# Optimization experiments

Hardware: AMD Instinct MI355X
Metric: run time of the kernel (lower is better)

The kernel has to match this reference:

```python
import jax, jax.numpy as jnp
import numpy as np

B, N, D, H = 256, 1000, 512, 8
HD = D // H


def _xavier(key, shape):
    # xavier_uniform-style init (bound = sqrt(6/(fan_in+fan_out)))
    bound = np.sqrt(6.0 / (shape[0] + shape[1])).astype(np.float32)
    return jax.random.uniform(key, shape, jnp.float32, -bound, bound)


def setup_inputs() -> dict:
    key = jax.random.key(0)
    ks = jax.random.split(key, 12)
    encoder_inputs = jax.random.normal(ks[0], (B, N, D), jnp.float32)
    pool = jax.random.normal(ks[1], (B, D), jnp.float32)
    dynamic_capacity = jax.random.uniform(ks[2], (B, 1), jnp.float32)
    mask = jax.random.randint(ks[3], (B, N), 0, 2).astype(jnp.int32)
    mask = mask.at[:, 0].set(0)  # depot always feasible -> MHA softmax well-defined
    return {
        'encoder_inputs': encoder_inputs,
        'pool': pool,
        'dynamic_capacity': dynamic_capacity,
        'mask': mask,
        'W_fc': _xavier(ks[4], (D + 1, D)),   # GAT_Decoder.fc (stored as [in,out])
        'W_fc1': _xavier(ks[5], (D, D)),      # GAT_Decoder.fc1
        'Wq': _xavier(ks[6], (D, D)),         # TransformerAttention.w (cat=1)
        'Wk_mha': _xavier(ks[7], (D, D)),     # TransformerAttention.k
        'Wv': _xavier(ks[8], (D, D)),         # TransformerAttention.v
        'Wo': _xavier(ks[9], (D, D)),         # TransformerAttention.fc
        'Wk_ptr': _xavier(ks[10], (D, D)),    # PointerAttention.k
    }


def reference(encoder_inputs, pool, dynamic_capacity, mask,
              W_fc, W_fc1, Wq, Wk_mha, Wv, Wo, Wk_ptr):
    T = 1.0
    norm_mha = np.float32(1.0 / np.sqrt(HD))
    norm_ptr = np.float32(1.0 / np.sqrt(D))
    mb = mask.astype(bool)                                   # [B,N]

    # --- one decode step of GAT_Decoder ---
    _input = encoder_inputs[:, 0, :]                          # [B,D]
    dec_in = jnp.concatenate([_input, dynamic_capacity], -1)  # [B,D+1]
    state = dec_in @ W_fc + pool @ W_fc1                      # [B,D] (fc + fc1(pool))

    # --- TransformerAttention (single-query masked MHA) ---
    Q = (state @ Wq).reshape(B, H, HD)                        # [B,H,hd]
    K = (encoder_inputs @ Wk_mha).reshape(B, N, H, HD)        # [B,N,H,hd]
    V = (encoder_inputs @ Wv).reshape(B, N, H, HD)
    compat = norm_mha * jnp.einsum('bhd,bnhd->bhn', Q, K)    # [B,H,N]
    u = jnp.where(mb[:, None, :], -jnp.inf, compat)
    attn = jax.nn.softmax(u, axis=-1)                         # [B,H,N]
    mha_out = jnp.einsum('bhn,bnhd->bhd', attn, V).reshape(B, D) @ Wo  # [B,D]

    # --- Pointer attention (tanh-clipped logits) ---
    Kp = encoder_inputs @ Wk_ptr                              # [B,N,D]
    compat2 = norm_ptr * jnp.einsum('bd,bnd->bn', mha_out, Kp)  # [B,N]
    x = jnp.tanh(compat2) * 10.0
    x = jnp.where(mb, -jnp.inf, x)
    all_masked = jnp.all(x == -jnp.inf, axis=-1, keepdims=True)
    x = jnp.where(all_masked, 0.0, x)                         # uniform fallback
    scores = jax.nn.softmax(x / T, axis=-1)                   # [B,N]
    return scores
```

## Files before the change

kernel.cpp:

```cpp
#include <hip/hip_runtime.h>
#include <cstdint>
#include <cstddef>

#define BB 256
#define NN 1000
#define DD 512
#define HH 8

__global__ __launch_bounds__(256) void k_state(
    const float* __restrict__ X, const float* __restrict__ pool,
    const float* __restrict__ cap, const float* __restrict__ Wfc,
    const float* __restrict__ Wfc1, float* __restrict__ state) {
  __shared__ float dec_lds[8][DD];
  __shared__ float pool_lds[8][DD];
  __shared__ float cap_lds[8];
  const int t = threadIdx.x;
  const int b0 = blockIdx.x * 8;
  for (int i = t; i < 8 * 128; i += 256) {
    int r = i >> 7, c4 = i & 127;
    ((float4*)dec_lds[r])[c4]  = ((const float4*)(X + (size_t)(b0 + r) * NN * DD))[c4];
    ((float4*)pool_lds[r])[c4] = ((const float4*)(pool + (size_t)(b0 + r) * DD))[c4];
  }
  if (t < 8) cap_lds[t] = cap[b0 + t];
  __syncthreads();
  const int e = blockIdx.y * 64 + (t & 63);
  const int g = t >> 6;
  const int r0 = g * 2, r1 = r0 + 1;
  float a0 = 0.f, a1 = 0.f;
  for (int d = 0; d < DD; ++d) {
    float w1 = Wfc[(size_t)d * DD + e];
    float w2 = Wfc1[(size_t)d * DD + e];
    a0 = fmaf(dec_lds[r0][d], w1, a0); a0 = fmaf(pool_lds[r0][d], w2, a0);
    a1 = fmaf(dec_lds[r1][d], w1, a1); a1 = fmaf(pool_lds[r1][d], w2, a1);
  }
  float wc = Wfc[(size_t)DD * DD + e];
  a0 += cap_lds[r0] * wc;
  a1 += cap_lds[r1] * wc;
  state[(size_t)(b0 + r0) * DD + e] = a0;
  state[(size_t)(b0 + r1) * DD + e] = a1;
}

__global__ __launch_bounds__(256) void k_qt(
    const float* __restrict__ state, const float* __restrict__ Wq,
    const float* __restrict__ Wk, float* __restrict__ Qt) {
  __shared__ float s_lds[8][DD];
  __shared__ float q_lds[8][64];
  __shared__ float wk_lds[64][65];
  const int t = threadIdx.x;
  const int b0 = blockIdx.x * 8;
  const int h = blockIdx.y;
  for (int i = t; i < 8 * 128; i += 256) {
    int r = i >> 7, c4 = i & 127;
    ((float4*)s_lds[r])[c4] = ((const float4*)(state + (size_t)(b0 + r) * DD))[c4];
  }
  __syncthreads();
  const int hd = t & 63;
  const int g = t >> 6;
  const int r0 = g * 2, r1 = r0 + 1;
  {
    float a0 = 0.f, a1 = 0.f;
    for (int e = 0; e < DD; ++e) {
      float w = Wq[(size_t)e * DD + h * 64 + hd];
      a0 = fmaf(s_lds[r0][e], w, a0);
      a1 = fmaf(s_lds[r1][e], w, a1);
    }
    q_lds[r0][hd] = a0;
    q_lds[r1][hd] = a1;
  }
  const float norm = 0.125f;
  for (int dc = 0; dc < DD; dc += 64) {
    __syncthreads();
    for (int i = t; i < 64 * 16; i += 256) {
      int row = i >> 4, c4 = i & 15;
      float4 wv = ((const float4*)(Wk + (size_t)(dc + row) * DD + h * 64))[c4];
      wk_lds[row][c4 * 4 + 0] = wv.x; wk_lds[row][c4 * 4 + 1] = wv.y;
      wk_lds[row][c4 * 4 + 2] = wv.z; wk_lds[row][c4 * 4 + 3] = wv.w;
    }
    __syncthreads();
    const int dl = t & 63;
    float a0 = 0.f, a1 = 0.f;
    for (int k = 0; k < 64; ++k) {
      float w = wk_lds[dl][k];
      a0 = fmaf(q_lds[r0][k], w, a0);
      a1 = fmaf(q_lds[r1][k], w, a1);
    }
    Qt[((size_t)(b0 + r0) * HH + h) * DD + dc + dl] = norm * a0;
    Qt[((size_t)(b0 + r1) * HH + h) * DD + dc + dl] = norm * a1;
  }
}

__global__ __launch_bounds__(256) void k_attn(
    const float* __restrict__ X, const int* __restrict__ mask,
    const float* __restrict__ Qt, float* __restrict__ ctx_out) {
  __shared__ float x_lds[16][516];
  __shared__ float qt_lds[HH][516];
  __shared__ float c_lds[16][9];
  __shared__ float w_lds[16][9];
  __shared__ float flag_lds[16];
  __shared__ float mml[HH], lsum[HH], alpha_lds[HH];

  const int t = threadIdx.x;
  const int b = blockIdx.x;
  const float* Xb = X + (size_t)b * NN * DD;

  for (int i = t; i < HH * 128; i += 256) {
    int r = i >> 7, c4 = i & 127;
    ((float4*)qt_lds[r])[c4] = ((const float4*)(Qt + ((size_t)b * HH + r) * DD))[c4];
  }
  if (t < HH) { mml[t] = -3e38f; lsum[t] = 0.f; }

  const int n2  = t >> 5;
  const int h4  = (t >> 4) & 1;
  const int dsl = t & 15;
  const int cr0 = n2 * 2, cr1 = cr0 + 1;
  const int hb = h4 * 4;
  const int chb = (t >> 7) * 4;
  const int dq  = t & 127;

  float4 ctxv0 = {0,0,0,0}, ctxv1 = {0,0,0,0}, ctxv2 = {0,0,0,0}, ctxv3 = {0,0,0,0};
  float4 pf[8];
  float mfl = 0.f;

  {
    #pragma unroll
    for (int k = 0; k < 8; ++k) {
      int fl = t + 256 * k;
      int r = fl >> 7, c4 = fl & 127;
      pf[k] = (r < NN) ? ((const float4*)(Xb + (size_t)r * DD))[c4]
                       : make_float4(0.f, 0.f, 0.f, 0.f);
    }
    if (t < 16) mfl = (t < NN && mask[(size_t)b * NN + t] == 0) ? 1.f : 0.f;
  }

  const int NT = (NN + 15) / 16;
  for (int it = 0; it < NT; ++it) {
    #pragma unroll
    for (int k = 0; k < 8; ++k) {
      int fl = t + 256 * k;
      int r = fl >> 7, c4 = fl & 127;
      ((float4*)x_lds[r])[c4] = pf[k];
    }
    if (t < 16) flag_lds[t] = mfl;
    __syncthreads();

    {
      const int n0 = (it + 1) * 16;
      #pragma unroll
      for (int k = 0; k < 8; ++k) {
        int fl = t + 256 * k;
        int r = fl >> 7, c4 = fl & 127;
        int n = n0 + r;
        pf[k] = (n < NN) ? ((const float4*)(Xb + (size_t)n * DD))[c4]
                         : make_float4(0.f, 0.f, 0.f, 0.f);
      }
      if (t < 16) {
        int n = n0 + t;
        mfl = (n < NN && mask[(size_t)b * NN + n] == 0) ? 1.f : 0.f;
      }
    }

    {
      float a00=0.f,a01=0.f,a02=0.f,a03=0.f;
      float a10=0.f,a11=0.f,a12=0.f,a13=0.f;
      #pragma unroll
      for (int k = 0; k < 8; ++k) {
        const int q = dsl + 16 * k;
        const float4 x0 = ((const float4*)x_lds[cr0])[q];
        const float4 x1 = ((const float4*)x_lds[cr1])[q];
        const float4 q0 = ((const float4*)qt_lds[hb + 0])[q];
        const float4 q1 = ((const float4*)qt_lds[hb + 1])[q];
        const float4 q2 = ((const float4*)qt_lds[hb + 2])[q];
        const float4 q3 = ((const float4*)qt_lds[hb + 3])[q];
        a00 += x0.x*q0.x + x0.y*q0.y + x0.z*q0.z + x0.w*q0.w;
        a01 += x0.x*q1.x + x0.y*q1.y + x0.z*q1.z + x0.w*q1.w;
        a02 += x0.x*q2.x + x0.y*q2.y + x0.z*q2.z + x0.w*q2.w;
        a03 += x0.x*q3.x + x0.y*q3.y + x0.z*q3.z + x0.w*q3.w;
        a10 += x1.x*q0.x + x1.y*q0.y + x1.z*q0.z + x1.w*q0.w;
        a11 += x1.x*q1.x + x1.y*q1.y + x1.z*q1.z + x1.w*q1.w;
        a12 += x1.x*q2.x + x1.y*q2.y + x1.z*q2.z + x1.w*q2.w;
        a13 += x1.x*q3.x + x1.y*q3.y + x1.z*q3.z + x1.w*q3.w;
      }
      #pragma unroll
      for (int mm = 1; mm < 16; mm <<= 1) {
        a00 += __shfl_xor(a00, mm); a01 += __shfl_xor(a01, mm);
        a02 += __shfl_xor(a02, mm); a03 += __shfl_xor(a03, mm);
        a10 += __shfl_xor(a10, mm); a11 += __shfl_xor(a11, mm);
        a12 += __shfl_xor(a12, mm); a13 += __shfl_xor(a13, mm);
      }
      if (dsl == 0) {
        const bool f0 = flag_lds[cr0] > 0.5f;
        const bool f1 = flag_lds[cr1] > 0.5f;
        c_lds[cr0][hb + 0] = f0 ? a00 : -3e38f;
        c_lds[cr0][hb + 1] = f0 ? a01 : -3e38f;
        c_lds[cr0][hb + 2] = f0 ? a02 : -3e38f;
        c_lds[cr0][hb + 3] = f0 ? a03 : -3e38f;
        c_lds[cr1][hb + 0] = f1 ? a10 : -3e38f;
        c_lds[cr1][hb + 1] = f1 ? a11 : -3e38f;
        c_lds[cr1][hb + 2] = f1 ? a12 : -3e38f;
        c_lds[cr1][hb + 3] = f1 ? a13 : -3e38f;
      }
    }
    __syncthreads();

    if (t < HH) {
      const int h = t;
      float m_old = mml[h];
      float tmax = -3e38f;
      #pragma unroll
      for (int n = 0; n < 16; ++n) tmax = fmaxf(tmax, c_lds[n][h]);
      float new_m = fmaxf(m_old, tmax);
      alpha_lds[h] = __expf(m_old - new_m);
      mml[h] = new_m;
    }
    __syncthreads();

    if (t < 128) {
      const int h = t >> 4, n = t & 15;
      float c = c_lds[n][h];
      float p = (flag_lds[n] > 0.5f) ? __expf(c - mml[h]) : 0.f;
      w_lds[n][h] = p;
      float s = p;
      #pragma unroll
      for (int mm = 1; mm < 16; mm <<= 1) s += __shfl_xor(s, mm);
      if (n == 0) lsum[h] = lsum[h] * alpha_lds[h] + s;
    }
    __syncthreads();

    {
      const float al0 = alpha_lds[chb + 0], al1 = alpha_lds[chb + 1];
      const float al2 = alpha_lds[chb + 2], al3 = alpha_lds[chb + 3];
      ctxv0.x *= al0; ctxv0.y *= al0; ctxv0.z *= al0; ctxv0.w *= al0;
      ctxv1.x *= al1; ctxv1.y *= al1; ctxv1.z *= al1; ctxv1.w *= al1;
      ctxv2.x *= al2; ctxv2.y *= al2; ctxv2.z *= al2; ctxv2.w *= al2;
      ctxv3.x *= al3; ctxv3.y *= al3; ctxv3.z *= al3; ctxv3.w *= al3;
      #pragma unroll
      for (int n = 0; n < 16; ++n) {
        const float4 xv = ((const float4*)x_lds[n])[dq];
        const float w0 = w_lds[n][chb + 0];
        const float w1 = w_lds[n][chb + 1];
        const float w2 = w_lds[n][chb + 2];
        const float w3 = w_lds[n][chb + 3];
        ctxv0.x += w0 * xv.x; ctxv0.y += w0 * xv.y; ctxv0.z += w0 * xv.z; ctxv0.w += w0 * xv.w;
        ctxv1.x += w1 * xv.x; ctxv1.y += w1 * xv.y; ctxv1.z += w1 * xv.z; ctxv1.w += w1 * xv.w;
        ctxv2.x += w2 * xv.x; ctxv2.y += w2 * xv.y; ctxv2.z += w2 * xv.z; ctxv2.w += w2 * xv.w;
        ctxv3.x += w3 * xv.x; ctxv3.y += w3 * xv.y; ctxv3.z += w3 * xv.z; ctxv3.w += w3 * xv.w;
      }
    }
    __syncthreads();
  }

  {
    const float i0 = 1.0f / lsum[chb + 0];
    const float i1 = 1.0f / lsum[chb + 1];
    const float i2 = 1.0f / lsum[chb + 2];
    const float i3 = 1.0f / lsum[chb + 3];
    float4 o;
    o = ctxv0; o.x *= i0; o.y *= i0; o.z *= i0; o.w *= i0;
    ((float4*)(ctx_out + ((size_t)b * HH + chb + 0) * DD))[dq] = o;
    o = ctxv1; o.x *= i1; o.y *= i1; o.z *= i1; o.w *= i1;
    ((float4*)(ctx_out + ((size_t)b * HH + chb + 1) * DD))[dq] = o;
    o = ctxv2; o.x *= i2; o.y *= i2; o.z *= i2; o.w *= i2;
    ((float4*)(ctx_out + ((size_t)b * HH + chb + 2) * DD))[dq] = o;
    o = ctxv3; o.x *= i3; o.y *= i3; o.z *= i3; o.w *= i3;
    ((float4*)(ctx_out + ((size_t)b * HH + chb + 3) * DD))[dq] = o;
  }
}

__global__ __launch_bounds__(256) void k_pre(
    const float* __restrict__ ctx, const float* __restrict__ Wv,
    float* __restrict__ pre) {
  __shared__ float c_lds[8][DD];
  const int t = threadIdx.x;
  const int b0 = blockIdx.x * 8;
  const int h = blockIdx.y;
  for (int i = t; i < 8 * 128; i += 256) {
    int r = i >> 7, c4 = i & 127;
    ((float4*)c_lds[r])[c4] =
        ((const float4*)(ctx + ((size_t)(b0 + r) * HH + h) * DD))[c4];
  }
  __syncthreads();
  const int hd = t & 63, g = t >> 6;
  const int r0 = g * 2, r1 = r0 + 1;
  float a0 = 0.f, a1 = 0.f;
  for (int d = 0; d < DD; ++d) {
    float w = Wv[(size_t)d * DD + h * 64 + hd];
    a0 = fmaf(c_lds[r0][d], w, a0);
    a1 = fmaf(c_lds[r1][d], w, a1);
  }
  pre[(size_t)(b0 + r0) * DD + h * 64 + hd] = a0;
  pre[(size_t)(b0 + r1) * DD + h * 64 + hd] = a1;
}

__global__ __launch_bounds__(256) void k_mo(
    const float* __restrict__ pre, const float* __restrict__ Wo,
    float* __restrict__ mo) {
  __shared__ float p_lds[8][DD];
  const int t = threadIdx.x;
  const int b0 = blockIdx.x * 8;
  const int c0 = blockIdx.y * 64;
  for (int i = t; i < 8 * 128; i += 256) {
    int r = i >> 7, c4 = i & 127;
    ((float4*)p_lds[r])[c4] = ((const float4*)(pre + (size_t)(b0 + r) * DD))[c4];
  }
  __syncthreads();
  const int c = c0 + (t & 63);
  const int g = t >> 6;
  const int r0 = g * 2, r1 = r0 + 1;
  float a0 = 0.f, a1 = 0.f;
  for (int e = 0; e < DD; ++e) {
    float w = Wo[(size_t)e * DD + c];
    a0 = fmaf(p_lds[r0][e], w, a0);
    a1 = fmaf(p_lds[r1][e], w, a1);
  }
  mo[(size_t)(b0 + r0) * DD + c] = a0;
  mo[(size_t)(b0 + r1) * DD + c] = a1;
}

__global__ __launch_bounds__(256) void k_scores(
    const float* __restrict__ X, const int* __restrict__ mask,
    const float* __restrict__ mo, const float* __restrict__ Wkp,
    float* __restrict__ out) {
  __shared__ float m_lds[DD];
  __shared__ float p_lds[DD];
  __shared__ float x_lds[16][516];
  __shared__ float xbuf[NN];
  __shared__ float red[16];
  const int t = threadIdx.x;
  const int b = blockIdx.x;
  const float* Xb = X + (size_t)b * NN * DD;

  ((float2*)m_lds)[t] = ((const float2*)(mo + (size_t)b * DD))[t];
  __syncthreads();
  {
    const float norm = 0.04419417382415922f;
    const float* w0 = Wkp + (size_t)t * DD;
    float a0 = 0.f;
    for (int e = 0; e < DD; e += 4) {
      float4 wa = *(const float4*)(w0 + e);
      a0 += wa.x * m_lds[e] + wa.y * m_lds[e + 1] + wa.z * m_lds[e + 2] + wa.w * m_lds[e + 3];
    }
    p_lds[t] = norm * a0;
    const float* w1 = Wkp + (size_t)(t + 256) * DD;
    float a1 = 0.f;
    for (int e = 0; e < DD; e += 4) {
      float4 wb = *(const float4*)(w1 + e);
      a1 += wb.x * m_lds[e] + wb.y * m_lds[e + 1] + wb.z * m_lds[e + 2] + wb.w * m_lds[e + 3];
    }
    p_lds[t + 256] = norm * a1;
  }
  __syncthreads();

  const int n = t >> 4, dsl = t & 15;
  float4 preg[8];
  #pragma unroll
  for (int k = 0; k < 8; ++k) preg[k] = ((const float4*)p_lds)[dsl + 16 * k];

  float4 pf[8];
  {
    #pragma unroll
    for (int k = 0; k < 8; ++k) {
      int fl = t + 256 * k;
      int r = fl >> 7, c4 = fl & 127;
      pf[k] = (r < NN) ? ((const float4*)(Xb + (size_t)r * DD))[c4]
                       : make_float4(0.f, 0.f, 0.f, 0.f);
    }
  }
  const int NT = (NN + 15) / 16;
  for (int it = 0; it < NT; ++it) {
    #pragma unroll
    for (int k = 0; k < 8; ++k) {
      int fl = t + 256 * k;
      int r = fl >> 7, c4 = fl & 127;
      ((float4*)x_lds[r])[c4] = pf[k];
    }
    __syncthreads();
    {
      const int n0 = (it + 1) * 16;
      #pragma unroll
      for (int k = 0; k < 8; ++k) {
        int fl = t + 256 * k;
        int r = fl >> 7, c4 = fl & 127;
        int nn = n0 + r;
        pf[k] = (nn < NN) ? ((const float4*)(Xb + (size_t)nn * DD))[c4]
                          : make_float4(0.f, 0.f, 0.f, 0.f);
      }
    }
    float y = 0.f;
    #pragma unroll
    for (int k = 0; k < 8; ++k) {
      const float4 xv = ((const float4*)x_lds[n])[dsl + 16 * k];
      y += xv.x * preg[k].x + xv.y * preg[k].y + xv.z * preg[k].z + xv.w * preg[k].w;
    }
    #pragma unroll
    for (int mm = 1; mm < 16; mm <<= 1) y += __shfl_xor(y, mm);
    if (dsl == 0) {
      const int nn = it * 16 + n;
      if (nn < NN) {
        bool valid = (mask[(size_t)b * NN + nn] == 0);
        xbuf[nn] = valid ? 10.f * tanhf(y) : -3e38f;
      }
    }
    __syncthreads();
  }

  float mx = -3e38f;
  for (int i = t; i < NN; i += 256) mx = fmaxf(mx, xbuf[i]);
  #pragma unroll
  for (int mm = 1; mm < 64; mm <<= 1) mx = fmaxf(mx, __shfl_xor(mx, mm));
  if ((t & 63) == 0) red[t >> 6] = mx;
  __syncthreads();
  if (t == 0) red[8] = fmaxf(fmaxf(red[0], red[1]), fmaxf(red[2], red[3]));
  __syncthreads();
  const float M = red[8];
  float s = 0.f;
  for (int i = t; i < NN; i += 256) s += __expf(xbuf[i] - M);
  #pragma unroll
  for (int mm = 1; mm < 64; mm <<= 1) s += __shfl_xor(s, mm);
  if ((t & 63) == 0) red[4 + (t >> 6)] = s;
  __syncthreads();
  if (t == 0) red[9] = 1.0f / (red[4] + red[5] + red[6] + red[7]);
  __syncthreads();
  const float invS = red[9];
  const bool uni = (M < -1e37f);
  for (int i = t; i < NN; i += 256)
    out[(size_t)b * NN + i] = uni ? (1.0f / NN) : __expf(xbuf[i] - M) * invS;
}

extern "C" void kernel_launch(void* const* d_in, const int* in_sizes, int n_in,
                              void* d_out, int out_size, void* d_ws, size_t ws_size,
                              hipStream_t stream) {
  const float* X    = (const float*)d_in[0];
  const float* pool = (const float*)d_in[1];
  const float* cap  = (const float*)d_in[2];
  const int*   mask = (const int*)d_in[3];
  const float* Wfc  = (const float*)d_in[4];
  const float* Wfc1 = (const float*)d_in[5];
  const float* Wq   = (const float*)d_in[6];
  const float* Wk   = (const float*)d_in[7];
  const float* Wv   = (const float*)d_in[8];
  const float* Wo   = (const float*)d_in[9];
  const float* Wkp  = (const float*)d_in[10];
  float* out = (float*)d_out;

  float* ws    = (float*)d_ws;
  float* state = ws;
  float* Qt    = state + BB * DD;
  float* ctx   = Qt + BB * HH * DD;
  float* pre   = ctx + BB * HH * DD;
  float* mo    = pre + BB * DD;

  k_state<<<dim3(32, 8), 256, 0, stream>>>(X, pool, cap, Wfc, Wfc1, state);
  k_qt<<<dim3(32, 8), 256, 0, stream>>>(state, Wq, Wk, Qt);
  k_attn<<<dim3(BB), 256, 0, stream>>>(X, mask, Qt, ctx);
  k_pre<<<dim3(32, 8), 256, 0, stream>>>(ctx, Wv, pre);
  k_mo<<<dim3(32, 8), 256, 0, stream>>>(pre, Wo, mo);
  k_scores<<<dim3(BB), 256, 0, stream>>>(X, mask, mo, Wkp, out);
}
```

Before: 1.095 ms.

## Split attention and pointer-logit passes over sequence chunks with separate merge kernels

The attention kernel is split into 3 blocks per batch along the sequence, each writing a partial context and its max/sum state, and the Wv projection kernel merges the three parts flash-decoding style. The pointer scoring is divided into a projection kernel, a logits kernel split 4-way over N, and a separate softmax kernel, with tanh computed via exp. The aim is to launch far more blocks than the 256-per-batch layout so the GPU's compute units are better filled during the X-streaming passes. It also keeps two Q rows in registers, merges the per-step max and exp phases to drop one barrier, and adds launch-bound occupancy hints, at the cost of extra workspace traffic and more kernel launches.

```diff
diff --git a/kernel.cpp b/kernel.cpp
--- a/kernel.cpp
+++ b/kernel.cpp
@@ -89,9 +89,10 @@
   }
 }
 
-__global__ __launch_bounds__(256) void k_attn(
+__global__ __launch_bounds__(256, 3) void k_attn(
     const float* __restrict__ X, const int* __restrict__ mask,
-    const float* __restrict__ Qt, float* __restrict__ ctx_out) {
+    const float* __restrict__ Qt, float* __restrict__ ctx_part,
+    float* __restrict__ ml_part) {
   __shared__ float x_lds[16][516];
   __shared__ float qt_lds[HH][516];
   __shared__ float c_lds[16][9];
@@ -100,8 +101,10 @@
   __shared__ float mml[HH], lsum[HH], alpha_lds[HH];
 
   const int t = threadIdx.x;
-  const int b = blockIdx.x;
+  const int s = blockIdx.x;
+  const int b = blockIdx.y;
   const float* Xb = X + (size_t)b * NN * DD;
+  const int t0 = s * 21, t1 = t0 + 21;
 
   for (int i = t; i < HH * 128; i += 256) {
     int r = i >> 7, c4 = i & 127;
@@ -109,9 +112,9 @@
   }
   if (t < HH) { mml[t] = -3e38f; lsum[t] = 0.f; }
 
+  const int dsl = t & 15;
   const int n2  = t >> 5;
   const int h4  = (t >> 4) & 1;
-  const int dsl = t & 15;
   const int cr0 = n2 * 2, cr1 = cr0 + 1;
   const int hb = h4 * 4;
   const int chb = (t >> 7) * 4;
@@ -122,18 +125,30 @@
   float mfl = 0.f;
 
   {
+    const int n0 = t0 * 16;
     #pragma unroll
     for (int k = 0; k < 8; ++k) {
       int fl = t + 256 * k;
       int r = fl >> 7, c4 = fl & 127;
-      pf[k] = (r < NN) ? ((const float4*)(Xb + (size_t)r * DD))[c4]
+      int n = n0 + r;
+      pf[k] = (n < NN) ? ((const float4*)(Xb + (size_t)n * DD))[c4]
                        : make_float4(0.f, 0.f, 0.f, 0.f);
     }
-    if (t < 16) mfl = (t < NN && mask[(size_t)b * NN + t] == 0) ? 1.f : 0.f;
-  }
-
-  const int NT = (NN + 15) / 16;
-  for (int it = 0; it < NT; ++it) {
+    if (t < 16) {
+      int n = n0 + t;
+      mfl = (n < NN && mask[(size_t)b * NN + n] == 0) ? 1.f : 0.f;
+    }
+  }
+  __syncthreads();
+
+  float4 qtr[16];
+  #pragma unroll
+  for (int k = 0; k < 8; ++k) {
+    qtr[2 * k]     = ((const float4*)qt_lds[hb + 0])[dsl + 16 * k];
+    qtr[2 * k + 1] = ((const float4*)qt_lds[hb + 1])[dsl + 16 * k];
+  }
+
+  for (int it = t0; it < t1; ++it) {
     #pragma unroll
     for (int k = 0; k < 8; ++k) {
       int fl = t + 256 * k;
@@ -150,12 +165,13 @@
         int fl = t + 256 * k;
         int r = fl >> 7, c4 = fl & 127;
         int n = n0 + r;
-        pf[k] = (n < NN) ? ((const float4*)(Xb + (size_t)n * DD))[c4]
-                         : make_float4(0.f, 0.f, 0.f, 0.f);
+        pf[k] = (it + 1 < t1 && n < NN)
+                    ? ((const float4*)(Xb + (size_t)n * DD))[c4]
+                    : make_float4(0.f, 0.f, 0.f, 0.f);
       }
       if (t < 16) {
         int n = n0 + t;
-        mfl = (n < NN && mask[(size_t)b * NN + n] == 0) ? 1.f : 0.f;
+        mfl = (it + 1 < t1 && n < NN && mask[(size_t)b * NN + n] == 0) ? 1.f : 0.f;
       }
     }
 
@@ -167,8 +183,8 @@
         const int q = dsl + 16 * k;
         const float4 x0 = ((const float4*)x_lds[cr0])[q];
         const float4 x1 = ((const float4*)x_lds[cr1])[q];
-        const float4 q0 = ((const float4*)qt_lds[hb + 0])[q];
-        const float4 q1 = ((const float4*)qt_lds[hb + 1])[q];
+        const float4 q0 = qtr[2 * k];
+        const float4 q1 = qtr[2 * k + 1];
         const float4 q2 = ((const float4*)qt_lds[hb + 2])[q];
         const float4 q3 = ((const float4*)qt_lds[hb + 3])[q];
         a00 += x0.x*q0.x + x0.y*q0.y + x0.z*q0.z + x0.w*q0.w;
@@ -202,27 +218,25 @@
     }
     __syncthreads();
 
-    if (t < HH) {
-      const int h = t;
-      float m_old = mml[h];
-      float tmax = -3e38f;
-      #pragma unroll
-      for (int n = 0; n < 16; ++n) tmax = fmaxf(tmax, c_lds[n][h]);
-      float new_m = fmaxf(m_old, tmax);
-      alpha_lds[h] = __expf(m_old - new_m);
-      mml[h] = new_m;
-    }
-    __syncthreads();
-
     if (t < 128) {
       const int h = t >> 4, n = t & 15;
       float c = c_lds[n][h];
-      float p = (flag_lds[n] > 0.5f) ? __expf(c - mml[h]) : 0.f;
+      float tmax = c;
+      #pragma unroll
+      for (int mm = 1; mm < 16; mm <<= 1) tmax = fmaxf(tmax, __shfl_xor(tmax, mm));
+      float m_old = mml[h];
+      float new_m = fmaxf(m_old, tmax);
+      float alpha = __expf(m_old - new_m);
+      float p = (c > -1e37f) ? __expf(c - new_m) : 0.f;
       w_lds[n][h] = p;
-      float s = p;
-      #pragma unroll
-      for (int mm = 1; mm < 16; mm <<= 1) s += __shfl_xor(s, mm);
-      if (n == 0) lsum[h] = lsum[h] * alpha_lds[h] + s;
+      float sum = p;
+      #pragma unroll
+      for (int mm = 1; mm < 16; mm <<= 1) sum += __shfl_xor(sum, mm);
+      if (n == 0) {
+        lsum[h] = lsum[h] * alpha + sum;
+        mml[h] = new_m;
+        alpha_lds[h] = alpha;
+      }
     }
     __syncthreads();
 
@@ -249,34 +263,52 @@
     __syncthreads();
   }
 
-  {
-    const float i0 = 1.0f / lsum[chb + 0];
-    const float i1 = 1.0f / lsum[chb + 1];
-    const float i2 = 1.0f / lsum[chb + 2];
-    const float i3 = 1.0f / lsum[chb + 3];
-    float4 o;
-    o = ctxv0; o.x *= i0; o.y *= i0; o.z *= i0; o.w *= i0;
-    ((float4*)(ctx_out + ((size_t)b * HH + chb + 0) * DD))[dq] = o;
-    o = ctxv1; o.x *= i1; o.y *= i1; o.z *= i1; o.w *= i1;
-    ((float4*)(ctx_out + ((size_t)b * HH + chb + 1) * DD))[dq] = o;
-    o = ctxv2; o.x *= i2; o.y *= i2; o.z *= i2; o.w *= i2;
-    ((float4*)(ctx_out + ((size_t)b * HH + chb + 2) * DD))[dq] = o;
-    o = ctxv3; o.x *= i3; o.y *= i3; o.z *= i3; o.w *= i3;
-    ((float4*)(ctx_out + ((size_t)b * HH + chb + 3) * DD))[dq] = o;
-  }
-}
-
-__global__ __launch_bounds__(256) void k_pre(
-    const float* __restrict__ ctx, const float* __restrict__ Wv,
-    float* __restrict__ pre) {
+  if (t < HH) {
+    size_t base = (((size_t)b * 3 + s) * HH + t) * 2;
+    ml_part[base + 0] = mml[t];
+    ml_part[base + 1] = lsum[t];
+  }
+  ((float4*)(ctx_part + (((size_t)b * 3 + s) * HH + chb + 0) * DD))[dq] = ctxv0;
+  ((float4*)(ctx_part + (((size_t)b * 3 + s) * HH + chb + 1) * DD))[dq] = ctxv1;
+  ((float4*)(ctx_part + (((size_t)b * 3 + s) * HH + chb + 2) * DD))[dq] = ctxv2;
+  ((float4*)(ctx_part + (((size_t)b * 3 + s) * HH + chb + 3) * DD))[dq] = ctxv3;
+}
+
+__global__ __launch_bounds__(256) void k_pre_merge(
+    const float* __restrict__ ctx_part, const float* __restrict__ ml_part,
+    const float* __restrict__ Wv, float* __restrict__ pre) {
   __shared__ float c_lds[8][DD];
+  __shared__ float wsplit[8][3];
   const int t = threadIdx.x;
   const int b0 = blockIdx.x * 8;
   const int h = blockIdx.y;
+  if (t < 8) {
+    const int b = b0 + t;
+    float m0 = ml_part[(((size_t)b * 3 + 0) * HH + h) * 2 + 0];
+    float l0 = ml_part[(((size_t)b * 3 + 0) * HH + h) * 2 + 1];
+    float m1 = ml_part[(((size_t)b * 3 + 1) * HH + h) * 2 + 0];
+    float l1 = ml_part[(((size_t)b * 3 + 1) * HH + h) * 2 + 1];
+    float m2 = ml_part[(((size_t)b * 3 + 2) * HH + h) * 2 + 0];
+    float l2 = ml_part[(((size_t)b * 3 + 2) * HH + h) * 2 + 1];
+    float M = fmaxf(m0, fmaxf(m1, m2));
+    float e0 = __expf(m0 - M), e1 = __expf(m1 - M), e2 = __expf(m2 - M);
+    float inv = 1.0f / (l0 * e0 + l1 * e1 + l2 * e2);
+    wsplit[t][0] = e0 * inv; wsplit[t][1] = e1 * inv; wsplit[t][2] = e2 * inv;
+  }
+  __syncthreads();
   for (int i = t; i < 8 * 128; i += 256) {
-    int r = i >> 7, c4 = i & 127;
-    ((float4*)c_lds[r])[c4] =
-        ((const float4*)(ctx + ((size_t)(b0 + r) * HH + h) * DD))[c4];
+    int r = i >> 7, q = i & 127;
+    const int b = b0 + r;
+    float4 p0 = ((const float4*)(ctx_part + (((size_t)b * 3 + 0) * HH + h) * DD))[q];
+    float4 p1 = ((const float4*)(ctx_part + (((size_t)b * 3 + 1) * HH + h) * DD))[q];
+    float4 p2 = ((const float4*)(ctx_part + (((size_t)b * 3 + 2) * HH + h) * DD))[q];
+    float w0 = wsplit[r][0], w1 = wsplit[r][1], w2 = wsplit[r][2];
+    float4 c;
+    c.x = w0 * p0.x + w1 * p1.x + w2 * p2.x;
+    c.y = w0 * p0.y + w1 * p1.y + w2 * p2.y;
+    c.z = w0 * p0.z + w1 * p1.z + w2 * p2.z;
+    c.w = w0 * p0.w + w1 * p1.w + w2 * p2.w;
+    ((float4*)c_lds[r])[q] = c;
   }
   __syncthreads();
   const int hd = t & 63, g = t >> 6;
@@ -316,57 +348,63 @@
   mo[(size_t)(b0 + r1) * DD + c] = a1;
 }
 
-__global__ __launch_bounds__(256) void k_scores(
+__global__ __launch_bounds__(256) void k_ptr(
+    const float* __restrict__ mo, const float* __restrict__ Wkp,
+    float* __restrict__ P) {
+  __shared__ float m_lds[DD];
+  const int t = threadIdx.x;
+  const int b = blockIdx.x;
+  ((float2*)m_lds)[t] = ((const float2*)(mo + (size_t)b * DD))[t];
+  __syncthreads();
+  const float norm = 0.04419417382415922f;
+  const float* w0 = Wkp + (size_t)t * DD;
+  float a0 = 0.f;
+  for (int e = 0; e < DD; e += 4) {
+    float4 wa = *(const float4*)(w0 + e);
+    a0 += wa.x * m_lds[e] + wa.y * m_lds[e+1] + wa.z * m_lds[e+2] + wa.w * m_lds[e+3];
+  }
+  P[(size_t)b * DD + t] = norm * a0;
+  const float* w1 = Wkp + (size_t)(t + 256) * DD;
+  float a1 = 0.f;
+  for (int e = 0; e < DD; e += 4) {
+    float4 wb = *(const float4*)(w1 + e);
+    a1 += wb.x * m_lds[e] + wb.y * m_lds[e+1] + wb.z * m_lds[e+2] + wb.w * m_lds[e+3];
+  }
+  P[(size_t)b * DD + t + 256] = norm * a1;
+}
+
+__global__ __launch_bounds__(256, 4) void k_logits(
     const float* __restrict__ X, const int* __restrict__ mask,
-    const float* __restrict__ mo, const float* __restrict__ Wkp,
-    float* __restrict__ out) {
-  __shared__ float m_lds[DD];
+    const float* __restrict__ P, float* __restrict__ logits) {
+  __shared__ float x_lds[16][516];
   __shared__ float p_lds[DD];
-  __shared__ float x_lds[16][516];
-  __shared__ float xbuf[NN];
-  __shared__ float red[16];
-  const int t = threadIdx.x;
-  const int b = blockIdx.x;
+  const int t = threadIdx.x;
+  const int s = blockIdx.x;
+  const int b = blockIdx.y;
   const float* Xb = X + (size_t)b * NN * DD;
-
-  ((float2*)m_lds)[t] = ((const float2*)(mo + (size_t)b * DD))[t];
-  __syncthreads();
-  {
-    const float norm = 0.04419417382415922f;
-    const float* w0 = Wkp + (size_t)t * DD;
-    float a0 = 0.f;
-    for (int e = 0; e < DD; e += 4) {
-      float4 wa = *(const float4*)(w0 + e);
-      a0 += wa.x * m_lds[e] + wa.y * m_lds[e + 1] + wa.z * m_lds[e + 2] + wa.w * m_lds[e + 3];
-    }
-    p_lds[t] = norm * a0;
-    const float* w1 = Wkp + (size_t)(t + 256) * DD;
-    float a1 = 0.f;
-    for (int e = 0; e < DD; e += 4) {
-      float4 wb = *(const float4*)(w1 + e);
-      a1 += wb.x * m_lds[e] + wb.y * m_lds[e + 1] + wb.z * m_lds[e + 2] + wb.w * m_lds[e + 3];
-    }
-    p_lds[t + 256] = norm * a1;
-  }
-  __syncthreads();
+  const int t0 = s * 16, t1 = (s == 3) ? 63 : (t0 + 16);
+
+  ((float2*)p_lds)[t] = ((const float2*)(P + (size_t)b * DD))[t];
 
   const int n = t >> 4, dsl = t & 15;
-  float4 preg[8];
-  #pragma unroll
-  for (int k = 0; k < 8; ++k) preg[k] = ((const float4*)p_lds)[dsl + 16 * k];
-
   float4 pf[8];
   {
+    const int n0 = t0 * 16;
     #pragma unroll
     for (int k = 0; k < 8; ++k) {
       int fl = t + 256 * k;
       int r = fl >> 7, c4 = fl & 127;
-      pf[k] = (r < NN) ? ((const float4*)(Xb + (size_t)r * DD))[c4]
-                       : make_float4(0.f, 0.f, 0.f, 0.f);
-    }
-  }
-  const int NT = (NN + 15) / 16;
-  for (int it = 0; it < NT; ++it) {
+      int nn = n0 + r;
+      pf[k] = (nn < NN) ? ((const float4*)(Xb + (size_t)nn * DD))[c4]
+                        : make_float4(0.f, 0.f, 0.f, 0.f);
+    }
+  }
+  __syncthreads();
+  float4 preg[8];
+  #pragma unroll
+  for (int k = 0; k < 8; ++k) preg[k] = ((const float4*)p_lds)[dsl + 16 * k];
+
+  for (int it = t0; it < t1; ++it) {
     #pragma unroll
     for (int k = 0; k < 8; ++k) {
       int fl = t + 256 * k;
@@ -381,8 +419,9 @@
         int fl = t + 256 * k;
         int r = fl >> 7, c4 = fl & 127;
         int nn = n0 + r;
-        pf[k] = (nn < NN) ? ((const float4*)(Xb + (size_t)nn * DD))[c4]
-                          : make_float4(0.f, 0.f, 0.f, 0.f);
+        pf[k] = (it + 1 < t1 && nn < NN)
+                    ? ((const float4*)(Xb + (size_t)nn * DD))[c4]
+                    : make_float4(0.f, 0.f, 0.f, 0.f);
       }
     }
     float y = 0.f;
@@ -397,14 +436,22 @@
       const int nn = it * 16 + n;
       if (nn < NN) {
         bool valid = (mask[(size_t)b * NN + nn] == 0);
-        xbuf[nn] = valid ? 10.f * tanhf(y) : -3e38f;
-      }
-    }
-    __syncthreads();
-  }
-
-  float mx = -3e38f;
-  for (int i = t; i < NN; i += 256) mx = fmaxf(mx, xbuf[i]);
+        float th = 1.0f - 2.0f / (__expf(2.0f * y) + 1.0f);
+        logits[(size_t)b * NN + nn] = valid ? 10.f * th : -3e38f;
+      }
+    }
+    __syncthreads();
+  }
+}
+
+__global__ __launch_bounds__(256) void k_softmax(
+    const float* __restrict__ logits, float* __restrict__ out) {
+  __shared__ float red[12];
+  const int t = threadIdx.x;
+  const int b = blockIdx.x;
+  const float4* lp = (const float4*)(logits + (size_t)b * NN);
+  float4 v = (t < 250) ? lp[t] : make_float4(-3e38f, -3e38f, -3e38f, -3e38f);
+  float mx = fmaxf(fmaxf(v.x, v.y), fmaxf(v.z, v.w));
   #pragma unroll
   for (int mm = 1; mm < 64; mm <<= 1) mx = fmaxf(mx, __shfl_xor(mx, mm));
   if ((t & 63) == 0) red[t >> 6] = mx;
@@ -412,18 +459,29 @@
   if (t == 0) red[8] = fmaxf(fmaxf(red[0], red[1]), fmaxf(red[2], red[3]));
   __syncthreads();
   const float M = red[8];
-  float s = 0.f;
-  for (int i = t; i < NN; i += 256) s += __expf(xbuf[i] - M);
+  float4 e;
+  e.x = (t < 250 && v.x > -1e37f) ? __expf(v.x - M) : 0.f;
+  e.y = (t < 250 && v.y > -1e37f) ? __expf(v.y - M) : 0.f;
+  e.z = (t < 250 && v.z > -1e37f) ? __expf(v.z - M) : 0.f;
+  e.w = (t < 250 && v.w > -1e37f) ? __expf(v.w - M) : 0.f;
+  float s = e.x + e.y + e.z + e.w;
   #pragma unroll
   for (int mm = 1; mm < 64; mm <<= 1) s += __shfl_xor(s, mm);
   if ((t & 63) == 0) red[4 + (t >> 6)] = s;
   __syncthreads();
-  if (t == 0) red[9] = 1.0f / (red[4] + red[5] + red[6] + red[7]);
-  __syncthreads();
-  const float invS = red[9];
+  if (t == 0) red[9] = red[4] + red[5] + red[6] + red[7];
+  __syncthreads();
+  const float S = red[9];
   const bool uni = (M < -1e37f);
-  for (int i = t; i < NN; i += 256)
-    out[(size_t)b * NN + i] = uni ? (1.0f / NN) : __expf(xbuf[i] - M) * invS;
+  const float invS = uni ? 0.f : 1.0f / S;
+  if (t < 250) {
+    float4 o;
+    o.x = uni ? (1.0f / NN) : e.x * invS;
+    o.y = uni ? (1.0f / NN) : e.y * invS;
+    o.z = uni ? (1.0f / NN) : e.z * invS;
+    o.w = uni ? (1.0f / NN) : e.w * invS;
+    ((float4*)(out + (size_t)b * NN))[t] = o;
+  }
 }
 
 extern "C" void kernel_launch(void* const* d_in, const int* in_sizes, int n_in,
@@ -442,17 +500,22 @@
   const float* Wkp  = (const float*)d_in[10];
   float* out = (float*)d_out;
 
-  float* ws    = (float*)d_ws;
-  float* state = ws;
-  float* Qt    = state + BB * DD;
-  float* ctx   = Qt + BB * HH * DD;
-  float* pre   = ctx + BB * HH * DD;
-  float* mo    = pre + BB * DD;
+  float* ws = (float*)d_ws;
+  float* state    = ws;
+  float* Qt       = state + BB * DD;
+  float* ctx_part = Qt + BB * HH * DD;
+  float* ml_part  = ctx_part + BB * 3 * HH * DD;
+  float* pre      = ml_part + BB * 3 * HH * 2;
+  float* mo       = pre + BB * DD;
+  float* P        = mo + BB * DD;
+  float* logits   = P + BB * DD;
 
   k_state<<<dim3(32, 8), 256, 0, stream>>>(X, pool, cap, Wfc, Wfc1, state);
   k_qt<<<dim3(32, 8), 256, 0, stream>>>(state, Wq, Wk, Qt);
-  k_attn<<<dim3(BB), 256, 0, stream>>>(X, mask, Qt, ctx);
-  k_pre<<<dim3(32, 8), 256, 0, stream>>>(ctx, Wv, pre);
+  k_attn<<<dim3(3, BB), 256, 0, stream>>>(X, mask, Qt, ctx_part, ml_part);
+  k_pre_merge<<<dim3(32, 8), 256, 0, stream>>>(ctx_part, ml_part, Wv, pre);
   k_mo<<<dim3(32, 8), 256, 0, stream>>>(pre, Wo, mo);
-  k_scores<<<dim3(BB), 256, 0, stream>>>(X, mask, mo, Wkp, out);
-}
+  k_ptr<<<dim3(BB), 256, 0, stream>>>(mo, Wkp, P);
+  k_logits<<<dim3(4, BB), 256, 0, stream>>>(X, mask, P, logits);
+  k_softmax<<<dim3(BB), 256, 0, stream>>>(logits, out);
+}
```

Measured after the change: 1.403 ms. 1.28x slower.
